# Kernel optimization log

Hardware: AMD Instinct MI355X
Metric: run time of the kernel (lower is better)

The kernel has to match this reference:

```python
import jax, jax.numpy as jnp
import numpy as np

D_MODEL = 768
D_STATE = 64
D_CONV = 4
D_INNER = 1536          # expand * d_model
HEADDIM = 64
NHEADS = D_INNER // HEADDIM  # 24
RANK = 8
SCALE = 16.0 / RANK     # lora alpha / rank = 2.0
D_IN_PROJ = 2 * D_INNER + 2 * D_STATE + NHEADS  # 3224
CONV_DIM = D_INNER + 2 * D_STATE                # 1664
EPS = 1e-6


def _rmsnorm(x, w):
    return x * jax.lax.rsqrt(jnp.mean(x * x, axis=-1, keepdims=True) + EPS) * w


def _loop_rope(x, loop_index):
    # per-loop-index RoPE: same rotation applied to every token/position
    inv_freq = 1.0 / (10000.0 ** (jnp.arange(0, D_MODEL, 2, dtype=jnp.float32) / D_MODEL))
    freqs = jnp.float32(loop_index) * inv_freq
    cos_v = jnp.repeat(jnp.cos(freqs), 2)[:D_MODEL].astype(x.dtype)
    sin_v = jnp.repeat(jnp.sin(freqs), 2)[:D_MODEL].astype(x.dtype)
    rot = jnp.stack([-x[..., 1::2], x[..., ::2]], axis=-1).reshape(x.shape)
    return x * cos_v + rot * sin_v


def _mamba2_core(x, in_base, lora_A_in, lora_B_in, conv_w, conv_b, dt_bias,
                 A_log, D_param, gated_norm_w, out_base, lora_A_out, lora_B_out):
    Bsz, L, _ = x.shape
    # LoRA-adapted input projection
    W_in = in_base + SCALE * (lora_B_in @ lora_A_in)          # (3224, 768)
    zxbcdt = x @ W_in.T                                       # (b, l, 3224)
    z = zxbcdt[..., :D_INNER]                                 # gate branch
    xBC = zxbcdt[..., D_INNER:D_INNER + CONV_DIM]             # conv branch
    dt = jax.nn.softplus(zxbcdt[..., -NHEADS:] + dt_bias)     # (b, l, h)
    # depthwise causal conv1d + silu
    xc = jax.lax.conv_general_dilated(
        xBC.transpose(0, 2, 1), conv_w[:, None, :], (1,), [(D_CONV - 1, 0)],
        dimension_numbers=('NCH', 'OIH', 'NCH'), feature_group_count=CONV_DIM)
    xBC = jax.nn.silu(xc.transpose(0, 2, 1) + conv_b)
    xs = xBC[..., :D_INNER].reshape(Bsz, L, NHEADS, HEADDIM)  # (b, l, h, p)
    Bm = xBC[..., D_INNER:D_INNER + D_STATE]                  # (b, l, n)
    Cm = xBC[..., D_INNER + D_STATE:]                         # (b, l, n)
    A = -jnp.exp(A_log)                                       # (h,)
    dA = jnp.exp(dt * A)                                      # (b, l, h)
    # sequential selective scan (same math as chunked SSD)
    def step(h, inp):
        dA_t, dt_t, B_t, C_t, x_t = inp
        h = dA_t[:, :, None, None] * h + jnp.einsum('bh,bn,bhp->bhpn', dt_t, B_t, x_t)
        y = jnp.einsum('bn,bhpn->bhp', C_t, h)
        return h, y
    tm = lambda a: jnp.moveaxis(a, 1, 0)  # time-major
    h0 = jnp.zeros((Bsz, NHEADS, HEADDIM, D_STATE), x.dtype)
    _, y = jax.lax.scan(step, h0, (tm(dA), tm(dt), tm(Bm), tm(Cm), tm(xs)))
    y = jnp.moveaxis(y, 0, 1) + D_param[None, None, :, None] * xs  # skip term
    y = y.reshape(Bsz, L, D_INNER)
    # gated RMSNorm (RMSNormGated): norm(y * silu(z))
    y = _rmsnorm(y * jax.nn.silu(z), gated_norm_w)
    # LoRA-adapted output projection
    W_out = out_base + SCALE * (lora_B_out @ lora_A_out)      # (768, 1536)
    return y @ W_out.T


def _forward(x, x_prompt, in_base, lora_A_in, lora_B_in, conv_w, conv_b, dt_bias,
             A_log, D_param, gated_norm_w, out_base, lora_A_out, lora_B_out,
             loop_norm_w, lifeline_gate, n_loops):
    for i in range(n_loops):
        h = _loop_rope(_rmsnorm(x, loop_norm_w), i)
        h = _mamba2_core(h, in_base, lora_A_in, lora_B_in, conv_w, conv_b, dt_bias,
                         A_log, D_param, gated_norm_w, out_base, lora_A_out, lora_B_out)
        x = h + lifeline_gate * x_prompt   # lifeline gated residual injection
    return x


def setup_inputs() -> dict:
    key = jax.random.key(0)
    ks = jax.random.split(key, 12)
    f32 = jnp.float32
    rn = lambda k, s, sc=0.02: jax.random.normal(k, s, dtype=f32) * sc
    return {
        'x': jax.random.normal(ks[0], (2, 1024, D_MODEL), f32),
        'x_prompt': jax.random.normal(ks[1], (2, 1024, D_MODEL), f32),
        'in_base': rn(ks[2], (D_IN_PROJ, D_MODEL)),
        'lora_A_in': rn(ks[3], (RANK, D_MODEL), 0.1),
        'lora_B_in': rn(ks[4], (D_IN_PROJ, RANK), 0.01),
        'conv_w': rn(ks[5], (CONV_DIM, D_CONV), 0.1),
        'conv_b': jnp.zeros((CONV_DIM,), f32),
        'dt_bias': rn(ks[6], (NHEADS,), 0.5),
        'A_log': jnp.log(jnp.linspace(1.0, 16.0, NHEADS, dtype=f32)),
        'D_param': jnp.ones((NHEADS,), f32),
        'gated_norm_w': jnp.ones((D_INNER,), f32),
        'out_base': rn(ks[7], (D_MODEL, D_INNER)),
        'lora_A_out': rn(ks[8], (RANK, D_INNER), 0.1),
        'lora_B_out': rn(ks[9], (D_MODEL, RANK), 0.01),
        'loop_norm_w': jnp.ones((D_MODEL,), f32),
        'lifeline_gate': jnp.ones((D_MODEL,), f32),
        'n_loops': 2,
    }


def reference(x, x_prompt, in_base, lora_A_in, lora_B_in, conv_w, conv_b, dt_bias,
              A_log, D_param, gated_norm_w, out_base, lora_A_out, lora_B_out,
              loop_norm_w, lifeline_gate, n_loops):
    return _forward(x, x_prompt, in_base, lora_A_in, lora_B_in, conv_w, conv_b, dt_bias,
                    A_log, D_param, gated_norm_w, out_base, lora_A_out, lora_B_out,
                    loop_norm_w, lifeline_gate, n_loops)
```

## Files before the change

### kernel.cpp

```cpp
#include <hip/hip_runtime.h>
#include <hip/hip_bf16.h>
#include <math.h>

#define D_MODEL 768
#define D_STATE 64
#define D_CONV 4
#define D_INNER 1536
#define HEADDIM 64
#define NHEADS 24
#define RANK 8
#define D_IN_PROJ 3224
#define NPAD 3328
#define ZSTR 3328
#define CONV_DIM 1664
#define BSZ 2
#define SEQ 1024
#define NROWS (BSZ*SEQ)
#define SCALE_LORA 2.0f
#define LC 64
#define NCHUNK (SEQ/LC)
#define LSTR 72

typedef __attribute__((ext_vector_type(8))) short bf16x8;
typedef __attribute__((ext_vector_type(4))) float f32x4;


__device__ inline float waveReduceSum(float v) {
#pragma unroll
    for (int m = 32; m; m >>= 1) v += __shfl_xor(v, m, 64);
    return v;
}

template <int NWAVES>
__device__ inline float blockReduceSum(float v) {
    __shared__ float tmp[NWAVES];
    int lane = threadIdx.x & 63, wid = threadIdx.x >> 6;
    v = waveReduceSum(v);
    if (lane == 0) tmp[wid] = v;
    __syncthreads();
    float tot = 0.f;
#pragma unroll
    for (int i = 0; i < NWAVES; i++) tot += tmp[i];
    return tot;
}

__device__ inline float sigmoidf_(float x) { return 1.f / (1.f + expf(-x)); }

__device__ inline unsigned short f2bf(float f) {
    union { float f; unsigned int u; } v; v.f = f;
    unsigned int r = (v.u + 0x7fffu + ((v.u >> 16) & 1u)) >> 16;
    return (unsigned short)r;
}

__device__ inline void load_lds16(const void* g, void* l) {
    __builtin_amdgcn_global_load_lds((const __attribute__((address_space(1))) void*)g,
                                     (__attribute__((address_space(3))) void*)l, 16, 0, 0);
}


__global__ void build_w_in_kernel(const float* __restrict__ base,
                                  const float* __restrict__ lA,
                                  const float* __restrict__ lB,
                                  unsigned short* __restrict__ W) {
    int idx = blockIdx.x * blockDim.x + threadIdx.x;
    if (idx >= NPAD * D_MODEL) return;
    int r = idx / D_MODEL, c = idx - r * D_MODEL;
    if (r >= D_IN_PROJ) { W[idx] = 0; return; }
    float s = 0.f;
#pragma unroll
    for (int k = 0; k < RANK; k++) s += lB[r * RANK + k] * lA[k * D_MODEL + c];
    W[idx] = f2bf(base[(size_t)r * D_MODEL + c] + SCALE_LORA * s);
}

__global__ void build_w_out_kernel(const float* __restrict__ base,
                                   const float* __restrict__ lA,
                                   const float* __restrict__ lB,
                                   unsigned short* __restrict__ W) {
    int idx = blockIdx.x * blockDim.x + threadIdx.x;
    if (idx >= D_MODEL * D_INNER) return;
    int r = idx / D_INNER, c = idx - r * D_INNER;
    float s = 0.f;
#pragma unroll
    for (int k = 0; k < RANK; k++) s += lB[r * RANK + k] * lA[k * D_INNER + c];
    W[idx] = f2bf(base[idx] + SCALE_LORA * s);
}

__global__ __launch_bounds__(384) void rmsrope_kernel(
    const float* __restrict__ x, const float* __restrict__ w,
    unsigned short* __restrict__ out, int loop_i) {
    int row = blockIdx.x;
    const float* xr = x + (size_t)row * D_MODEL;
    int j = threadIdx.x;
    float x0 = xr[2 * j], x1 = xr[2 * j + 1];
    float ss = blockReduceSum<6>(x0 * x0 + x1 * x1);
    float sc = rsqrtf(ss * (1.f / D_MODEL) + 1e-6f);
    float y0 = x0 * sc * w[2 * j];
    float y1 = x1 * sc * w[2 * j + 1];
    float ang = (float)loop_i * expf((float)(2 * j) * (-9.210340371976184f / (float)D_MODEL));
    float c = cosf(ang), sn = sinf(ang);
    unsigned short* orow = out + (size_t)row * D_MODEL;
    orow[2 * j]     = f2bf(y0 * c - y1 * sn);
    orow[2 * j + 1] = f2bf(y1 * c + y0 * sn);
}

__global__ __launch_bounds__(256) void gemm_bf16_kernel(
    const unsigned short* __restrict__ A,
    const unsigned short* __restrict__ B,
    float* __restrict__ C, int M, int N, int K, int Cstride,
    const float* __restrict__ xp, const float* __restrict__ gate) {
    __shared__ unsigned short lsA[128 * 64];
    __shared__ unsigned short lsB[128 * 64];
    int t = threadIdx.x;
    int w = t >> 6, lane = t & 63;
    int n0 = blockIdx.x * 128, m0 = blockIdx.y * 128;
    int wr = w >> 1, wc = w & 1;
    f32x4 acc[4][4];
#pragma unroll
    for (int i = 0; i < 4; i++)
#pragma unroll
        for (int j = 0; j < 4; j++) acc[i][j] = (f32x4){0.f, 0.f, 0.f, 0.f};

    for (int k0 = 0; k0 < K; k0 += 64) {
        __syncthreads();
#pragma unroll
        for (int o = 0; o < 4; o++) {
            int s = o * 256 + t;
            int row = s >> 3, colE = (s & 7) << 3;
            const unsigned short* ga = &A[(size_t)(m0 + row) * K + k0 + colE];
            const unsigned short* gb = &B[(size_t)(n0 + row) * K + k0 + colE];
            unsigned short* la = &lsA[(size_t)(o * 256 + (t & ~63)) * 8];
            unsigned short* lb = &lsB[(size_t)(o * 256 + (t & ~63)) * 8];
            load_lds16(ga, la);
            load_lds16(gb, lb);
        }
        __syncthreads();
#pragma unroll
        for (int kk = 0; kk < 2; kk++) {
            bf16x8 af[4], bfr[4];
            int kof = kk * 32 + (lane >> 4) * 8;
#pragma unroll
            for (int i = 0; i < 4; i++) {
                int row = wr * 64 + i * 16 + (lane & 15);
                af[i] = *(const bf16x8*)&lsA[row * 64 + kof];
            }
#pragma unroll
            for (int j = 0; j < 4; j++) {
                int row = wc * 64 + j * 16 + (lane & 15);
                bfr[j] = *(const bf16x8*)&lsB[row * 64 + kof];
            }
#pragma unroll
            for (int i = 0; i < 4; i++)
#pragma unroll
                for (int j = 0; j < 4; j++)
                    acc[i][j] = __builtin_amdgcn_mfma_f32_16x16x32_bf16(af[i], bfr[j], acc[i][j], 0, 0, 0);
        }
    }
#pragma unroll
    for (int i = 0; i < 4; i++) {
#pragma unroll
        for (int j = 0; j < 4; j++) {
#pragma unroll
            for (int r = 0; r < 4; r++) {
                int row = m0 + wr * 64 + i * 16 + (lane >> 4) * 4 + r;
                int col = n0 + wc * 64 + j * 16 + (lane & 15);
                float v = acc[i][j][r];
                if (gate) v += gate[col] * xp[(size_t)row * Cstride + col];
                C[(size_t)row * Cstride + col] = v;
            }
        }
    }
}

__global__ void conv_kernel(const float* __restrict__ zx, const float* __restrict__ cw,
                            const float* __restrict__ cb, float* __restrict__ xbc) {
    int idx = blockIdx.x * blockDim.x + threadIdx.x;
    if (idx >= BSZ * SEQ * CONV_DIM) return;
    int c = idx % CONV_DIM;
    int l = (idx / CONV_DIM) % SEQ;
    int b = idx / (CONV_DIM * SEQ);
    const float* base = zx + (size_t)b * SEQ * ZSTR + D_INNER + c;
    float acc = cb[c];
#pragma unroll
    for (int t = 0; t < 4; t++) {
        int ll = l - 3 + t;
        if (ll >= 0) acc = fmaf(cw[c * 4 + t], base[(size_t)ll * ZSTR], acc);
    }
    xbc[idx] = acc * sigmoidf_(acc);
}

__global__ __launch_bounds__(256) void scan_mfma_kernel(
    const float* __restrict__ xbc,
    const float* __restrict__ zx,
    const float* __restrict__ dt_bias,
    const float* __restrict__ A_log,
    const float* __restrict__ Dp,
    float* __restrict__ y,
    float* __restrict__ Fbuf,
    float* __restrict__ cumA) {
    __shared__ unsigned short Cc[64][LSTR];
    __shared__ unsigned short Bb[64][LSTR];
    __shared__ unsigned short Xt[64][LSTR];
    __shared__ unsigned short Bw[64][LSTR];
    __shared__ unsigned short Mm[64][LSTR];
    __shared__ float s_lds[64];
    __shared__ float dt_lds[64];

    int blk = blockIdx.x;
    int c = blk % NCHUNK;
    int bh = blk / NCHUNK;
    int h = bh % NHEADS, b = bh / NHEADS;
    int tid = threadIdx.x;
    int w = tid >> 6, lane = tid & 63;
    const int t0 = c * LC;

    if (w == 0) {
        int t = lane;
        size_t row = (size_t)(b * SEQ + t0 + t);
        float raw = zx[row * ZSTR + (D_INNER + CONV_DIM) + h] + dt_bias[h];
        float dt_t = raw > 20.f ? raw : log1pf(expf(raw));
        float s = dt_t * (-expf(A_log[h]));
#pragma unroll
        for (int off = 1; off < 64; off <<= 1) {
            float v = __shfl_up(s, off, 64);
            if (lane >= off) s += v;
        }
        s_lds[t] = s;
        dt_lds[t] = dt_t;
        cumA[(size_t)blk * LC + t] = expf(s);
    }

    float breg[16];
#pragma unroll
    for (int k = 0; k < 16; k++) {
        int idx = k * 256 + tid;
        int r = idx >> 6, ci = idx & 63;
        size_t row = (size_t)(b * SEQ + t0 + r) * CONV_DIM;
        float cv = xbc[row + D_INNER + D_STATE + ci];
        float bv = xbc[row + D_INNER + ci];
        float xv = xbc[row + h * HEADDIM + ci];
        Cc[r][ci] = f2bf(cv);
        Bb[r][ci] = f2bf(bv);
        Xt[ci][r] = f2bf(xv);
        breg[k] = bv;
    }
    __syncthreads();

    float s63 = s_lds[63];
#pragma unroll
    for (int k = 0; k < 16; k++) {
        int idx = k * 256 + tid;
        int r = idx >> 6, ci = idx & 63;
        float wu = expf(s63 - s_lds[r]) * dt_lds[r];
        Bw[ci][r] = f2bf(breg[k] * wu);
    }

    f32x4 accG[4];
#pragma unroll
    for (int j = 0; j < 4; j++) accG[j] = (f32x4){0.f, 0.f, 0.f, 0.f};
#pragma unroll
    for (int kk = 0; kk < 2; kk++) {
        int kof = kk * 32 + (lane >> 4) * 8;
        bf16x8 afr = *(const bf16x8*)&Cc[16 * w + (lane & 15)][kof];
#pragma unroll
        for (int j = 0; j < 4; j++) {
            bf16x8 bfr = *(const bf16x8*)&Bb[16 * j + (lane & 15)][kof];
            accG[j] = __builtin_amdgcn_mfma_f32_16x16x32_bf16(afr, bfr, accG[j], 0, 0, 0);
        }
    }
#pragma unroll
    for (int j = 0; j < 4; j++) {
#pragma unroll
        for (int r = 0; r < 4; r++) {
            int t = 16 * w + (lane >> 4) * 4 + r;
            int u = 16 * j + (lane & 15);
            float v = 0.f;
            if (u <= t) v = accG[j][r] * dt_lds[u] * expf(s_lds[t] - s_lds[u]);
            Mm[t][u] = f2bf(v);
        }
    }
    __syncthreads();

    f32x4 accY[4];
#pragma unroll
    for (int j = 0; j < 4; j++) accY[j] = (f32x4){0.f, 0.f, 0.f, 0.f};
#pragma unroll
    for (int kk = 0; kk < 2; kk++) {
        int kof = kk * 32 + (lane >> 4) * 8;
        bf16x8 afr = *(const bf16x8*)&Mm[16 * w + (lane & 15)][kof];
#pragma unroll
        for (int j = 0; j < 4; j++) {
            bf16x8 bfr = *(const bf16x8*)&Xt[16 * j + (lane & 15)][kof];
            accY[j] = __builtin_amdgcn_mfma_f32_16x16x32_bf16(afr, bfr, accY[j], 0, 0, 0);
        }
    }
    float D_h = Dp[h];
#pragma unroll
    for (int j = 0; j < 4; j++) {
#pragma unroll
        for (int r = 0; r < 4; r++) {
            int t = 16 * w + (lane >> 4) * 4 + r;
            int p = 16 * j + (lane & 15);
            size_t row = (size_t)(b * SEQ + t0 + t);
            float xv = xbc[row * CONV_DIM + h * HEADDIM + p];
            y[row * D_INNER + h * HEADDIM + p] = accY[j][r] + D_h * xv;
        }
    }

    f32x4 accF[4];
#pragma unroll
    for (int j = 0; j < 4; j++) accF[j] = (f32x4){0.f, 0.f, 0.f, 0.f};
#pragma unroll
    for (int kk = 0; kk < 2; kk++) {
        int kof = kk * 32 + (lane >> 4) * 8;
        bf16x8 afr = *(const bf16x8*)&Bw[16 * w + (lane & 15)][kof];
#pragma unroll
        for (int j = 0; j < 4; j++) {
            bf16x8 bfr = *(const bf16x8*)&Xt[16 * j + (lane & 15)][kof];
            accF[j] = __builtin_amdgcn_mfma_f32_16x16x32_bf16(afr, bfr, accF[j], 0, 0, 0);
        }
    }
#pragma unroll
    for (int j = 0; j < 4; j++) {
#pragma unroll
        for (int r = 0; r < 4; r++) {
            int n = 16 * w + (lane >> 4) * 4 + r;
            int p = 16 * j + (lane & 15);
            Fbuf[(size_t)blk * (HEADDIM * D_STATE) + n * HEADDIM + p] = accF[j][r];
        }
    }
}

__global__ __launch_bounds__(256) void combine_kernel(
    const float* __restrict__ Fbuf, const float* __restrict__ cumA,
    float* __restrict__ Hinit) {
    int bh = blockIdx.x;
    int tid = threadIdx.x;
    float H[16];
#pragma unroll
    for (int k = 0; k < 16; k++) H[k] = 0.f;
    for (int c = 0; c < NCHUNK; c++) {
        size_t base = (size_t)(bh * NCHUNK + c) * (HEADDIM * D_STATE);
        float pA = cumA[(size_t)(bh * NCHUNK + c) * LC + (LC - 1)];
#pragma unroll
        for (int k = 0; k < 16; k++) {
            size_t idx = base + tid + k * 256;
            Hinit[idx] = H[k];
            H[k] = fmaf(pA, H[k], Fbuf[idx]);
        }
    }
}

__global__ __launch_bounds__(256) void ycorr_kernel(
    const float* __restrict__ xbc, const float* __restrict__ cumA,
    const float* __restrict__ Hinit, float* __restrict__ y) {
    int blk = blockIdx.x;
    int c = blk % NCHUNK;
    int bh = blk / NCHUNK;
    int h = bh % NHEADS, b = bh / NHEADS;
    __shared__ float Cd[LC][D_STATE + 1];
    __shared__ float Hs[D_STATE][HEADDIM + 1];
    int tid = threadIdx.x;
    size_t cbase = (size_t)blk * LC;
    size_t hbase = (size_t)blk * (HEADDIM * D_STATE);
#pragma unroll
    for (int k = 0; k < 16; k++) {
        int idx = tid + k * 256;
        int r = idx >> 6, n = idx & 63;
        size_t row = (size_t)(b * SEQ + c * LC + r);
        Cd[r][n] = xbc[row * CONV_DIM + D_INNER + D_STATE + n] * cumA[cbase + r];
        Hs[r][n] = Hinit[hbase + idx];
    }
    __syncthreads();
    int tx = tid & 15, ty = tid >> 4;
    float acc[4][4] = {};
    for (int n = 0; n < D_STATE; n++) {
        float cv[4], hv[4];
#pragma unroll
        for (int i = 0; i < 4; i++) cv[i] = Cd[ty * 4 + i][n];
#pragma unroll
        for (int j = 0; j < 4; j++) hv[j] = Hs[n][tx * 4 + j];
#pragma unroll
        for (int i = 0; i < 4; i++)
#pragma unroll
            for (int j = 0; j < 4; j++)
                acc[i][j] = fmaf(cv[i], hv[j], acc[i][j]);
    }
#pragma unroll
    for (int i = 0; i < 4; i++) {
        int tt = ty * 4 + i;
        size_t row = (size_t)(b * SEQ + c * LC + tt);
#pragma unroll
        for (int j = 0; j < 4; j++) {
            int p = tx * 4 + j;
            size_t oidx = row * D_INNER + h * HEADDIM + p;
            y[oidx] += acc[i][j];
        }
    }
}

__global__ __launch_bounds__(256) void gatenorm_kernel(
    const float* __restrict__ y, const float* __restrict__ zx,
    const float* __restrict__ w, unsigned short* __restrict__ out) {
    int row = blockIdx.x;
    const float* z = zx + (size_t)row * ZSTR;
    const float* yr = y + (size_t)row * D_INNER;
    float g[6];
    float ss = 0.f;
#pragma unroll
    for (int e = 0; e < 6; e++) {
        int idx = threadIdx.x + e * 256;
        float zv = z[idx];
        float gv = yr[idx] * (zv * sigmoidf_(zv));
        g[e] = gv;
        ss += gv * gv;
    }
    ss = blockReduceSum<4>(ss);
    float sc = rsqrtf(ss * (1.f / D_INNER) + 1e-6f);
#pragma unroll
    for (int e = 0; e < 6; e++) {
        int idx = threadIdx.x + e * 256;
        out[(size_t)row * D_INNER + idx] = f2bf(g[e] * sc * w[idx]);
    }
}

extern "C" void kernel_launch(void* const* d_in, const int* in_sizes, int n_in,
                              void* d_out, int out_size, void* d_ws, size_t ws_size,
                              hipStream_t stream) {
    const float* x        = (const float*)d_in[0];
    const float* x_prompt = (const float*)d_in[1];
    const float* in_base  = (const float*)d_in[2];
    const float* lA_in    = (const float*)d_in[3];
    const float* lB_in    = (const float*)d_in[4];
    const float* conv_w   = (const float*)d_in[5];
    const float* conv_b   = (const float*)d_in[6];
    const float* dt_bias  = (const float*)d_in[7];
    const float* A_log    = (const float*)d_in[8];
    const float* D_param  = (const float*)d_in[9];
    const float* gnw      = (const float*)d_in[10];
    const float* out_base = (const float*)d_in[11];
    const float* lA_out   = (const float*)d_in[12];
    const float* lB_out   = (const float*)d_in[13];
    const float* loop_nw  = (const float*)d_in[14];
    const float* gate     = (const float*)d_in[15];
    float* out = (float*)d_out;

    float* ws_f = (float*)d_ws;
    float* zx    = ws_f;
    float* xbc   = zx    + (size_t)NROWS * ZSTR;
    float* ybuf  = xbc   + (size_t)NROWS * CONV_DIM;
    float* Fbuf  = ybuf  + (size_t)NROWS * D_INNER;
    float* Hinit = Fbuf  + (size_t)BSZ * NHEADS * NCHUNK * HEADDIM * D_STATE;
    float* cumA  = Hinit + (size_t)BSZ * NHEADS * NCHUNK * HEADDIM * D_STATE;
    unsigned short* W_in  = (unsigned short*)(cumA + (size_t)BSZ * NHEADS * NCHUNK * LC);
    unsigned short* W_out = W_in  + (size_t)NPAD * D_MODEL;
    unsigned short* hbuf  = W_out + (size_t)D_MODEL * D_INNER;
    unsigned short* ygt   = hbuf  + (size_t)NROWS * D_MODEL;

    build_w_in_kernel<<<(NPAD * D_MODEL + 255) / 256, 256, 0, stream>>>(in_base, lA_in, lB_in, W_in);
    build_w_out_kernel<<<(D_MODEL * D_INNER + 255) / 256, 256, 0, stream>>>(out_base, lA_out, lB_out, W_out);

    for (int i = 0; i < 2; i++) {
        const float* xsrc = (i == 0) ? x : out;
        rmsrope_kernel<<<NROWS, 384, 0, stream>>>(xsrc, loop_nw, hbuf, i);

        dim3 g1(NPAD / 128, NROWS / 128);
        gemm_bf16_kernel<<<g1, 256, 0, stream>>>(hbuf, W_in, zx, NROWS, NPAD, D_MODEL, ZSTR,
                                                 nullptr, nullptr);

        conv_kernel<<<(BSZ * SEQ * CONV_DIM + 255) / 256, 256, 0, stream>>>(zx, conv_w, conv_b, xbc);

        scan_mfma_kernel<<<BSZ * NHEADS * NCHUNK, 256, 0, stream>>>(
            xbc, zx, dt_bias, A_log, D_param, ybuf, Fbuf, cumA);
        combine_kernel<<<BSZ * NHEADS, 256, 0, stream>>>(Fbuf, cumA, Hinit);
        ycorr_kernel<<<BSZ * NHEADS * NCHUNK, 256, 0, stream>>>(xbc, cumA, Hinit, ybuf);

        gatenorm_kernel<<<NROWS, 256, 0, stream>>>(ybuf, zx, gnw, ygt);

        dim3 g2(D_MODEL / 128, NROWS / 128);
        gemm_bf16_kernel<<<g2, 256, 0, stream>>>(ygt, W_out, out, NROWS, D_MODEL, D_INNER, D_MODEL,
                                                 x_prompt, gate);
    }
}
```

Baseline: 384.8 us.

## Double-buffer GEMM with swizzled LDS, split-K out-proj, parallelize combine

The GEMM now double-buffers its LDS tiles so the next K-slice loads while MFMAs run on the current one. It also XOR-swizzles the LDS layout to reduce bank conflicts. The output projection uses 4-way split-K with atomicAdd into a buffer pre-filled by a new epilogue kernel holding gate*x_prompt, which raises block count from 96 to 384. The combine kernel is spread over 16x more blocks with one state element per thread. In exchange there are float atomics with nondeterministic summation order, an extra launch, and twice the LDS use.

```diff
diff --git a/kernel.cpp b/kernel.cpp
--- a/kernel.cpp
+++ b/kernel.cpp
@@ -103,16 +103,17 @@
     orow[2 * j + 1] = f2bf(y1 * c + y0 * sn);
 }
 
-__global__ __launch_bounds__(256) void gemm_bf16_kernel(
+__global__ __launch_bounds__(256) void gemm_pipe_kernel(
     const unsigned short* __restrict__ A,
     const unsigned short* __restrict__ B,
     float* __restrict__ C, int M, int N, int K, int Cstride,
-    const float* __restrict__ xp, const float* __restrict__ gate) {
-    __shared__ unsigned short lsA[128 * 64];
-    __shared__ unsigned short lsB[128 * 64];
+    int Ks, int mode) {
+    __shared__ unsigned short lsA[2][128 * 64];
+    __shared__ unsigned short lsB[2][128 * 64];
     int t = threadIdx.x;
     int w = t >> 6, lane = t & 63;
     int n0 = blockIdx.x * 128, m0 = blockIdx.y * 128;
+    int kbase = blockIdx.z * Ks;
     int wr = w >> 1, wc = w & 1;
     f32x4 acc[4][4];
 #pragma unroll
@@ -120,33 +121,40 @@
 #pragma unroll
         for (int j = 0; j < 4; j++) acc[i][j] = (f32x4){0.f, 0.f, 0.f, 0.f};
 
-    for (int k0 = 0; k0 < K; k0 += 64) {
-        __syncthreads();
-#pragma unroll
-        for (int o = 0; o < 4; o++) {
-            int s = o * 256 + t;
-            int row = s >> 3, colE = (s & 7) << 3;
-            const unsigned short* ga = &A[(size_t)(m0 + row) * K + k0 + colE];
-            const unsigned short* gb = &B[(size_t)(n0 + row) * K + k0 + colE];
-            unsigned short* la = &lsA[(size_t)(o * 256 + (t & ~63)) * 8];
-            unsigned short* lb = &lsB[(size_t)(o * 256 + (t & ~63)) * 8];
-            load_lds16(ga, la);
-            load_lds16(gb, lb);
-        }
-        __syncthreads();
+#define STAGE(bi, kk0)                                                           \
+    {                                                                            \
+        _Pragma("unroll")                                                        \
+        for (int o = 0; o < 4; o++) {                                            \
+            int s = o * 256 + t;                                                 \
+            int row = s >> 3, u = s & 7;                                         \
+            int usrc = (u ^ (row & 7)) << 3;                                     \
+            unsigned short* la = &lsA[bi][(size_t)(o * 256 + (t & ~63)) * 8];    \
+            unsigned short* lb = &lsB[bi][(size_t)(o * 256 + (t & ~63)) * 8];    \
+            load_lds16(&A[(size_t)(m0 + row) * K + (kk0) + usrc], la);           \
+            load_lds16(&B[(size_t)(n0 + row) * K + (kk0) + usrc], lb);           \
+        }                                                                        \
+    }
+
+    int nk = Ks >> 6;
+    STAGE(0, kbase);
+    __syncthreads();
+    int cur = 0;
+    for (int ks = 0; ks < nk; ks++) {
+        if (ks + 1 < nk) STAGE(cur ^ 1, kbase + (ks + 1) * 64);
 #pragma unroll
         for (int kk = 0; kk < 2; kk++) {
             bf16x8 af[4], bfr[4];
-            int kof = kk * 32 + (lane >> 4) * 8;
+            int u_t = kk * 4 + (lane >> 4);
+            int kof = (u_t ^ (lane & 7)) << 3;
 #pragma unroll
             for (int i = 0; i < 4; i++) {
                 int row = wr * 64 + i * 16 + (lane & 15);
-                af[i] = *(const bf16x8*)&lsA[row * 64 + kof];
+                af[i] = *(const bf16x8*)&lsA[cur][row * 64 + kof];
             }
 #pragma unroll
             for (int j = 0; j < 4; j++) {
                 int row = wc * 64 + j * 16 + (lane & 15);
-                bfr[j] = *(const bf16x8*)&lsB[row * 64 + kof];
+                bfr[j] = *(const bf16x8*)&lsB[cur][row * 64 + kof];
             }
 #pragma unroll
             for (int i = 0; i < 4; i++)
@@ -154,7 +162,11 @@
                 for (int j = 0; j < 4; j++)
                     acc[i][j] = __builtin_amdgcn_mfma_f32_16x16x32_bf16(af[i], bfr[j], acc[i][j], 0, 0, 0);
         }
-    }
+        __syncthreads();
+        cur ^= 1;
+    }
+#undef STAGE
+
 #pragma unroll
     for (int i = 0; i < 4; i++) {
 #pragma unroll
@@ -164,11 +176,23 @@
                 int row = m0 + wr * 64 + i * 16 + (lane >> 4) * 4 + r;
                 int col = n0 + wc * 64 + j * 16 + (lane & 15);
                 float v = acc[i][j][r];
-                if (gate) v += gate[col] * xp[(size_t)row * Cstride + col];
-                C[(size_t)row * Cstride + col] = v;
+                if (mode) atomicAdd(&C[(size_t)row * Cstride + col], v);
+                else      C[(size_t)row * Cstride + col] = v;
             }
         }
     }
+}
+
+__global__ void epilog_init_kernel(const float* __restrict__ xp,
+                                   const float* __restrict__ gate,
+                                   float* __restrict__ out) {
+    int idx = blockIdx.x * blockDim.x + threadIdx.x;
+    if (idx >= NROWS * D_MODEL / 4) return;
+    float4 xv = ((const float4*)xp)[idx];
+    int n0 = (idx * 4) % D_MODEL;
+    float4 g = *(const float4*)&gate[n0];
+    float4 o = make_float4(g.x * xv.x, g.y * xv.y, g.z * xv.z, g.w * xv.w);
+    ((float4*)out)[idx] = o;
 }
 
 __global__ void conv_kernel(const float* __restrict__ zx, const float* __restrict__ cw,
@@ -333,20 +357,15 @@
 __global__ __launch_bounds__(256) void combine_kernel(
     const float* __restrict__ Fbuf, const float* __restrict__ cumA,
     float* __restrict__ Hinit) {
-    int bh = blockIdx.x;
-    int tid = threadIdx.x;
-    float H[16];
-#pragma unroll
-    for (int k = 0; k < 16; k++) H[k] = 0.f;
+    int bh = blockIdx.x >> 4;
+    int np = (blockIdx.x & 15) * 256 + threadIdx.x;
+    float H = 0.f;
+#pragma unroll
     for (int c = 0; c < NCHUNK; c++) {
-        size_t base = (size_t)(bh * NCHUNK + c) * (HEADDIM * D_STATE);
+        size_t idx = (size_t)(bh * NCHUNK + c) * (HEADDIM * D_STATE) + np;
         float pA = cumA[(size_t)(bh * NCHUNK + c) * LC + (LC - 1)];
-#pragma unroll
-        for (int k = 0; k < 16; k++) {
-            size_t idx = base + tid + k * 256;
-            Hinit[idx] = H[k];
-            H[k] = fmaf(pA, H[k], Fbuf[idx]);
-        }
+        Hinit[idx] = H;
+        H = fmaf(pA, H, Fbuf[idx]);
     }
 }
 
@@ -463,21 +482,22 @@
         const float* xsrc = (i == 0) ? x : out;
         rmsrope_kernel<<<NROWS, 384, 0, stream>>>(xsrc, loop_nw, hbuf, i);
 
-        dim3 g1(NPAD / 128, NROWS / 128);
-        gemm_bf16_kernel<<<g1, 256, 0, stream>>>(hbuf, W_in, zx, NROWS, NPAD, D_MODEL, ZSTR,
-                                                 nullptr, nullptr);
+        dim3 g1(NPAD / 128, NROWS / 128, 1);
+        gemm_pipe_kernel<<<g1, 256, 0, stream>>>(hbuf, W_in, zx, NROWS, NPAD, D_MODEL, ZSTR,
+                                                 D_MODEL, 0);
 
         conv_kernel<<<(BSZ * SEQ * CONV_DIM + 255) / 256, 256, 0, stream>>>(zx, conv_w, conv_b, xbc);
 
         scan_mfma_kernel<<<BSZ * NHEADS * NCHUNK, 256, 0, stream>>>(
             xbc, zx, dt_bias, A_log, D_param, ybuf, Fbuf, cumA);
-        combine_kernel<<<BSZ * NHEADS, 256, 0, stream>>>(Fbuf, cumA, Hinit);
+        combine_kernel<<<BSZ * NHEADS * 16, 256, 0, stream>>>(Fbuf, cumA, Hinit);
         ycorr_kernel<<<BSZ * NHEADS * NCHUNK, 256, 0, stream>>>(xbc, cumA, Hinit, ybuf);
 
         gatenorm_kernel<<<NROWS, 256, 0, stream>>>(ybuf, zx, gnw, ygt);
 
-        dim3 g2(D_MODEL / 128, NROWS / 128);
-        gemm_bf16_kernel<<<g2, 256, 0, stream>>>(ygt, W_out, out, NROWS, D_MODEL, D_INNER, D_MODEL,
-                                                 x_prompt, gate);
-    }
-}
+        epilog_init_kernel<<<(NROWS * D_MODEL / 4 + 255) / 256, 256, 0, stream>>>(x_prompt, gate, out);
+        dim3 g2(D_MODEL / 128, NROWS / 128, 4);
+        gemm_pipe_kernel<<<g2, 256, 0, stream>>>(ygt, W_out, out, NROWS, D_MODEL, D_INNER, D_MODEL,
+                                                 D_INNER / 4, 1);
+    }
+}
```

After: 327.7 us. 1.17x faster.
